# Kernel tuning notes

Measured on AMD Instinct MI355X. Metric: run time of the kernel, lower is better.

The kernel has to match this reference:

```python
import jax, jax.numpy as jnp
import numpy as np

N = 50000   # nodes
E = 800000  # edges (before self-loops)
D = 256     # hidden_dim
H = 8       # heads
C = D // H  # 32 channels per head
NEG_SLOPE = 0.2


def setup_inputs() -> dict:
    key = jax.random.key(0)
    ks = jax.random.split(key, 10)
    sc = 0.05
    x = jax.random.normal(ks[0], (N, D), dtype=jnp.float32)
    edges_idx = jax.random.randint(ks[1], (2, E), 0, N, dtype=jnp.int64)
    # GATv2Conv params per layer: lin_l (W for source j), lin_r (W for target i), att [H,C], bias [H*C]
    Wl1 = jax.random.normal(ks[2], (D, H * C), dtype=jnp.float32) * sc
    Wr1 = jax.random.normal(ks[3], (D, H * C), dtype=jnp.float32) * sc
    att1 = jax.random.normal(ks[4], (H, C), dtype=jnp.float32) * sc
    b1 = jnp.zeros((H * C,), dtype=jnp.float32)
    Wl2 = jax.random.normal(ks[5], (D, H * C), dtype=jnp.float32) * sc
    Wr2 = jax.random.normal(ks[6], (D, H * C), dtype=jnp.float32) * sc
    att2 = jax.random.normal(ks[7], (H, C), dtype=jnp.float32) * sc
    b2 = jnp.zeros((H * C,), dtype=jnp.float32)
    return dict(x=x, edges_idx=edges_idx, Wl1=Wl1, Wr1=Wr1, att1=att1, b1=b1,
                Wl2=Wl2, Wr2=Wr2, att2=att2, b2=b2)


def gatv2_layer(x, src, dst, Wl, Wr, att, b):
    # x: [N, D]; src/dst: [E'] (self-loops included)
    xl = (x @ Wl).reshape(-1, H, C)  # source-side transform
    xr = (x @ Wr).reshape(-1, H, C)  # target-side transform
    # GATv2 score: e_ij = a^T LeakyReLU(Wl x_j + Wr x_i)
    z = jax.nn.leaky_relu(xl[src] + xr[dst], NEG_SLOPE)   # [E', H, C]
    e = jnp.einsum('ehc,hc->eh', z, att)                  # [E', H]
    # softmax over edges sharing the same target node (segment softmax)
    m = jax.ops.segment_max(e, dst, num_segments=N)       # [N, H]
    ex = jnp.exp(e - m[dst])
    s = jax.ops.segment_sum(ex, dst, num_segments=N)      # [N, H]
    alpha = ex / s[dst]                                   # [E', H]
    out = jax.ops.segment_sum(alpha[..., None] * xl[src], dst, num_segments=N)  # [N, H, C]
    return out.reshape(-1, H * C) + b


def reference(x, edges_idx, Wl1, Wr1, att1, b1, Wl2, Wr2, att2, b2):
    # PyG default add_self_loops=True
    loop = jnp.arange(N, dtype=edges_idx.dtype)
    src = jnp.concatenate([edges_idx[0], loop])
    dst = jnp.concatenate([edges_idx[1], loop])
    # layer 1 -> ELU -> layer 2 (dropout identity in eval mode)
    h = jax.nn.elu(gatv2_layer(x, src, dst, Wl1, Wr1, att1, b1))
    return gatv2_layer(h, src, dst, Wl2, Wr2, att2, b2)
```

## Files before the change

### kernel.cpp

```cpp
#include <hip/hip_runtime.h>
#include <hip/hip_bf16.h>
#include <math.h>

#define HEADS 8
#define HC 256
#define NEG_SLOPE 0.2f

typedef __attribute__((ext_vector_type(8))) short short8;
typedef __attribute__((ext_vector_type(16))) float floatx16;

__device__ inline ushort bf16_rne(float f) {
    unsigned u = __float_as_uint(f);
    return (ushort)((u + 0x7FFFu + ((u >> 16) & 1u)) >> 16);
}
__device__ inline float bf2f(ushort u) {
    return __uint_as_float(((unsigned)u) << 16);
}

__global__ __launch_bounds__(256) void cvt_bf16_sw(
        const float* __restrict__ x, ushort* __restrict__ xb, long long nblk) {
    long long id = (long long)blockIdx.x * blockDim.x + threadIdx.x;
    if (id >= nblk) return;
    long long r = id >> 5;
    int j = (int)(id & 31);
    const float4* p = (const float4*)(x + id * 8);
    float4 a = p[0], b = p[1];
    short8 pk;
    pk[0] = (short)bf16_rne(a.x); pk[1] = (short)bf16_rne(a.y);
    pk[2] = (short)bf16_rne(a.z); pk[3] = (short)bf16_rne(a.w);
    pk[4] = (short)bf16_rne(b.x); pk[5] = (short)bf16_rne(b.y);
    pk[6] = (short)bf16_rne(b.z); pk[7] = (short)bf16_rne(b.w);
    int jx = j ^ ((int)r & 7);
    *(short8*)(xb + r * 256 + jx * 8) = pk;
}

__global__ __launch_bounds__(256) void build_wt(
        const float* __restrict__ Wl, const float* __restrict__ Wr,
        ushort* __restrict__ wt) {
    int n = blockIdx.x;
    int k = threadIdx.x;
    const float* W = (n < 256) ? Wl : Wr;
    int col = n & 255;
    int jx = (k >> 3) ^ (n & 7);
    wt[n * HC + jx * 8 + (k & 7)] = bf16_rne(W[k * HC + col]);
}

__global__ __launch_bounds__(256) void gemm_mfma(
        const ushort* __restrict__ A, const ushort* __restrict__ wt,
        ushort* __restrict__ xl, ushort* __restrict__ xr, int N) {
    __shared__ ushort lA[64 * 256];
    __shared__ ushort lB[64 * 256];
    int nt = blockIdx.x & 7;
    int mt = blockIdx.x >> 3;
    int m0 = mt * 64, n0 = nt * 64;
    int t = threadIdx.x;
    int lane = t & 63, wv = t >> 6;

    {
        const ushort* gA = A + (long long)m0 * HC;
        const ushort* gB = wt + (long long)n0 * HC;
        #pragma unroll
        for (int i = 0; i < 8; ++i) {
            int off = (wv * 8 + i) * 512;
            __builtin_amdgcn_global_load_lds(
                (const __attribute__((address_space(1))) unsigned int*)(gA + off + lane * 8),
                (__attribute__((address_space(3))) unsigned int*)(lA + off), 16, 0, 0);
            __builtin_amdgcn_global_load_lds(
                (const __attribute__((address_space(1))) unsigned int*)(gB + off + lane * 8),
                (__attribute__((address_space(3))) unsigned int*)(lB + off), 16, 0, 0);
        }
    }
    __syncthreads();

    int rA = (wv & 1) * 32 + (lane & 31);
    int rB = (wv >> 1) * 32 + (lane & 31);
    int kh = lane >> 5;
    int sA = rA & 7, sB = rB & 7;
    floatx16 acc;
    #pragma unroll
    for (int i = 0; i < 16; ++i) acc[i] = 0.f;
    #pragma unroll
    for (int step = 0; step < 16; ++step) {
        int j = step * 2 + kh;
        short8 a = *(const short8*)&lA[rA * 256 + ((j ^ sA) * 8)];
        short8 b = *(const short8*)&lB[rB * 256 + ((j ^ sB) * 8)];
        acc = __builtin_amdgcn_mfma_f32_32x32x16_bf16(a, b, acc, 0, 0, 0);
    }

    ushort* obase = (nt < 4) ? xl : xr;
    int colb = (n0 & 255) + (wv >> 1) * 32 + (lane & 31);
    int rbase = m0 + (wv & 1) * 32 + 4 * kh;
    #pragma unroll
    for (int g = 0; g < 4; ++g) {
        #pragma unroll
        for (int q = 0; q < 4; ++q) {
            int row = rbase + q + 8 * g;
            if (row < N)
                obase[(long long)row * HC + colb] = bf16_rne(acc[g * 4 + q]);
        }
    }
}

__global__ void hist_dst(const int* __restrict__ eidx, int E, int N,
                         int* __restrict__ counts) {
    int w = blockIdx.x * blockDim.x + threadIdx.x;
    int Etot = E + N;
    if (w >= Etot) return;
    int d = (w < E) ? eidx[E + w] : (w - E);
    atomicAdd(&counts[d], 1);
}

__global__ __launch_bounds__(1024) void scan_local(
        const int* __restrict__ counts, int* __restrict__ rowptr,
        int* __restrict__ bsum, int N) {
    __shared__ int wsums[16];
    int t = threadIdx.x, lane = t & 63, wv = t >> 6;
    int i = blockIdx.x * 1024 + t;
    int v = (i < N) ? counts[i] : 0;
    int orig = v;
    #pragma unroll
    for (int off = 1; off < 64; off <<= 1) {
        int n = __shfl_up(v, off, 64);
        if (lane >= off) v += n;
    }
    if (lane == 63) wsums[wv] = v;
    __syncthreads();
    int woff = 0, total = 0;
    #pragma unroll
    for (int w_ = 0; w_ < 16; ++w_) {
        int s = wsums[w_];
        if (w_ < wv) woff += s;
        total += s;
    }
    if (i < N) rowptr[i] = v + woff - orig;
    if (t == 0) bsum[blockIdx.x] = total;
}

__global__ void scan_bsums(const int* __restrict__ bsum, int* __restrict__ bsum2,
                           int* __restrict__ rowptr, int nb, int N) {
    int lane = threadIdx.x;
    int v = (lane < nb) ? bsum[lane] : 0;
    int orig = v;
    #pragma unroll
    for (int off = 1; off < 64; off <<= 1) {
        int n = __shfl_up(v, off, 64);
        if (lane >= off) v += n;
    }
    if (lane < nb) bsum2[lane] = v - orig;
    if (lane == 63) rowptr[N] = v;
}

__global__ __launch_bounds__(1024) void scan_add(
        int* __restrict__ rowptr, const int* __restrict__ bsum2, int N) {
    int i = blockIdx.x * 1024 + threadIdx.x;
    if (i < N) rowptr[i] += bsum2[blockIdx.x];
}

__global__ void scatter_edges(const int* __restrict__ eidx, int E, int N,
                              const int* __restrict__ rowptr,
                              int* __restrict__ fill, int* __restrict__ srcS) {
    int w = blockIdx.x * blockDim.x + threadIdx.x;
    int Etot = E + N;
    if (w >= Etot) return;
    int s, d;
    if (w < E) { s = eidx[w]; d = eidx[E + w]; }
    else       { s = w - E;   d = w - E; }
    int pos = rowptr[d] + atomicAdd(&fill[d], 1);
    srcS[pos] = s;
}

template <int LAYER1>
__global__ __launch_bounds__(256) void gat_node(
        const ushort* __restrict__ xl, const ushort* __restrict__ xr,
        const float* __restrict__ att, const float* __restrict__ bias,
        const int* __restrict__ rowptr, const int* __restrict__ srcS,
        void* __restrict__ outp, int N) {
    int node = blockIdx.x * 4 + (threadIdx.x >> 6);
    int lane = threadIdx.x & 63;
    if (node >= N) return;
    int half = lane >> 5;
    int l = lane & 31;
    int beg = rowptr[node], end = rowptr[node + 1];

    short8 xu = *(const short8*)(xr + (long long)node * HC + l * 8);
    float xv[8];
    #pragma unroll
    for (int c = 0; c < 8; ++c) xv[c] = bf2f((ushort)xu[c]);
    const float4* ap = (const float4*)(att + l * 8);
    float4 a0 = ap[0], a1 = ap[1];
    float av[8] = {a0.x, a0.y, a0.z, a0.w, a1.x, a1.y, a1.z, a1.w};

    float ss = 0.f;
    float acc[8];
    #pragma unroll
    for (int c = 0; c < 8; ++c) acc[c] = 0.f;

    for (int p = beg + half; p < end; p += 2) {
        int s = srcS[p];
        short8 u = *(const short8*)(xl + (long long)s * HC + l * 8);
        float v[8];
        float st0 = 0.f, st1 = 0.f, sa0 = 0.f, sa1 = 0.f;
        #pragma unroll
        for (int c = 0; c < 4; ++c) {
            v[c] = bf2f((ushort)u[c]);
            float tt = v[c] + xv[c];
            st0 = fmaf(av[c], tt, st0);
            sa0 = fmaf(av[c], fabsf(tt), sa0);
        }
        #pragma unroll
        for (int c = 4; c < 8; ++c) {
            v[c] = bf2f((ushort)u[c]);
            float tt = v[c] + xv[c];
            st1 = fmaf(av[c], tt, st1);
            sa1 = fmaf(av[c], fabsf(tt), sa1);
        }
        float part = 0.6f * (st0 + st1) + 0.4f * (sa0 + sa1);
        part += __shfl_xor(part, 1, 64);
        part += __shfl_xor(part, 2, 64);
        float ex = __expf(part);
        ss += ex;
        #pragma unroll
        for (int c = 0; c < 8; ++c) acc[c] = fmaf(ex, v[c], acc[c]);
    }

    ss += __shfl_xor(ss, 32, 64);
    #pragma unroll
    for (int c = 0; c < 8; ++c) acc[c] += __shfl_xor(acc[c], 32, 64);

    float inv = 1.f / ss;
    const float4* bp = (const float4*)(bias + l * 8);
    float4 b0 = bp[0], b1 = bp[1];
    float bb[8] = {b0.x, b0.y, b0.z, b0.w, b1.x, b1.y, b1.z, b1.w};
    float o[8];
    #pragma unroll
    for (int c = 0; c < 8; ++c) o[c] = acc[c] * inv + bb[c];

    if (half == 0) {
        if (LAYER1) {
            short8 pk;
            #pragma unroll
            for (int c = 0; c < 8; ++c) {
                float e = o[c] > 0.f ? o[c] : expm1f(o[c]);
                pk[c] = (short)bf16_rne(e);
            }
            int jx = l ^ (node & 7);
            *(short8*)((ushort*)outp + (long long)node * HC + jx * 8) = pk;
        } else {
            float* po = (float*)outp + (long long)node * HC + l * 8;
            *(float4*)po = make_float4(o[0], o[1], o[2], o[3]);
            *(float4*)(po + 4) = make_float4(o[4], o[5], o[6], o[7]);
        }
    }
}

extern "C" void kernel_launch(void* const* d_in, const int* in_sizes, int n_in,
                              void* d_out, int out_size, void* d_ws, size_t ws_size,
                              hipStream_t stream) {
    const float* x    = (const float*)d_in[0];
    const int*   eidx = (const int*)d_in[1];
    const float* Wl1  = (const float*)d_in[2];
    const float* Wr1  = (const float*)d_in[3];
    const float* att1 = (const float*)d_in[4];
    const float* b1   = (const float*)d_in[5];
    const float* Wl2  = (const float*)d_in[6];
    const float* Wr2  = (const float*)d_in[7];
    const float* att2 = (const float*)d_in[8];
    const float* b2   = (const float*)d_in[9];
    float* out = (float*)d_out;

    const int N = in_sizes[0] / HC;
    const int E = in_sizes[1] / 2;
    const int Etot = E + N;
    const long long NHC = (long long)N * HC;

    ushort* xl   = (ushort*)d_ws;
    ushort* xr   = xl + NHC;
    ushort* hbuf = xr + NHC;
    ushort* xb   = hbuf + NHC;
    ushort* wt1  = xb + NHC;
    ushort* wt2  = wt1 + 512 * HC;
    int* rowptr  = (int*)(wt2 + 512 * HC);
    int* counts  = rowptr + (N + 1);
    int* fill    = counts + N;
    int* bsum    = fill + N;
    int* bsum2   = bsum + 64;
    int* srcS    = bsum2 + 64;

    const int TB = 256;
    dim3 blk(TB);
    int gEdgesT = (Etot + TB - 1) / TB;
    int gGemm   = ((N + 63) / 64) * 8;
    int gNode   = (N + 3) / 4;
    int nb      = (N + 1023) / 1024;
    long long nblk = NHC / 8;
    int gCvt    = (int)((nblk + TB - 1) / TB);

    cvt_bf16_sw<<<gCvt, blk, 0, stream>>>(x, xb, nblk);
    build_wt<<<512, blk, 0, stream>>>(Wl1, Wr1, wt1);
    build_wt<<<512, blk, 0, stream>>>(Wl2, Wr2, wt2);
    hipMemsetAsync(counts, 0, (size_t)2 * N * sizeof(int), stream);
    hist_dst<<<gEdgesT, blk, 0, stream>>>(eidx, E, N, counts);
    scan_local<<<nb, 1024, 0, stream>>>(counts, rowptr, bsum, N);
    scan_bsums<<<1, 64, 0, stream>>>(bsum, bsum2, rowptr, nb, N);
    scan_add<<<nb, 1024, 0, stream>>>(rowptr, bsum2, N);
    scatter_edges<<<gEdgesT, blk, 0, stream>>>(eidx, E, N, rowptr, fill, srcS);

    gemm_mfma<<<gGemm, blk, 0, stream>>>(xb, wt1, xl, xr, N);
    gat_node<1><<<gNode, blk, 0, stream>>>(xl, xr, att1, b1, rowptr, srcS, hbuf, N);

    gemm_mfma<<<gGemm, blk, 0, stream>>>(hbuf, wt2, xl, xr, N);
    gat_node<0><<<gNode, blk, 0, stream>>>(xl, xr, att2, b2, rowptr, srcS, out, N);
}
```

Measured before the change: 457.1 us.

## Process each node with full wave per edge and regroup GEMM tile order

The node aggregation kernel now has all 64 lanes cover one edge row with 4 channels each, instead of two half-waves each handling alternate edges with 8 channels. Edges are unrolled by two with independent accumulators, and the cross-half shuffle reduction is removed. The GEMM block mapping is regrouped so 16 consecutive M-tiles share an N-tile within a 128-block group, aimed at better L2 reuse of weight tiles. The GEMM change relies on the M-tile guard inside the kernel, since the padded grid now launches extra tiles past N.

```diff
diff --git a/kernel.cpp b/kernel.cpp
--- a/kernel.cpp
+++ b/kernel.cpp
@@ -50,8 +50,10 @@
         ushort* __restrict__ xl, ushort* __restrict__ xr, int N) {
     __shared__ ushort lA[64 * 256];
     __shared__ ushort lB[64 * 256];
-    int nt = blockIdx.x & 7;
-    int mt = blockIdx.x >> 3;
+    int local = blockIdx.x & 127;
+    int grp   = blockIdx.x >> 7;
+    int mt = grp * 16 + (local & 15);
+    int nt = local >> 4;
     int m0 = mt * 64, n0 = nt * 64;
     int t = threadIdx.x;
     int lane = t & 63, wv = t >> 6;
@@ -178,78 +180,68 @@
     int node = blockIdx.x * 4 + (threadIdx.x >> 6);
     int lane = threadIdx.x & 63;
     if (node >= N) return;
-    int half = lane >> 5;
-    int l = lane & 31;
     int beg = rowptr[node], end = rowptr[node + 1];
 
-    short8 xu = *(const short8*)(xr + (long long)node * HC + l * 8);
-    float xv[8];
-    #pragma unroll
-    for (int c = 0; c < 8; ++c) xv[c] = bf2f((ushort)xu[c]);
-    const float4* ap = (const float4*)(att + l * 8);
-    float4 a0 = ap[0], a1 = ap[1];
-    float av[8] = {a0.x, a0.y, a0.z, a0.w, a1.x, a1.y, a1.z, a1.w};
-
-    float ss = 0.f;
-    float acc[8];
-    #pragma unroll
-    for (int c = 0; c < 8; ++c) acc[c] = 0.f;
-
-    for (int p = beg + half; p < end; p += 2) {
-        int s = srcS[p];
-        short8 u = *(const short8*)(xl + (long long)s * HC + l * 8);
-        float v[8];
-        float st0 = 0.f, st1 = 0.f, sa0 = 0.f, sa1 = 0.f;
-        #pragma unroll
-        for (int c = 0; c < 4; ++c) {
-            v[c] = bf2f((ushort)u[c]);
-            float tt = v[c] + xv[c];
-            st0 = fmaf(av[c], tt, st0);
-            sa0 = fmaf(av[c], fabsf(tt), sa0);
-        }
-        #pragma unroll
-        for (int c = 4; c < 8; ++c) {
-            v[c] = bf2f((ushort)u[c]);
-            float tt = v[c] + xv[c];
-            st1 = fmaf(av[c], tt, st1);
-            sa1 = fmaf(av[c], fabsf(tt), sa1);
-        }
-        float part = 0.6f * (st0 + st1) + 0.4f * (sa0 + sa1);
-        part += __shfl_xor(part, 1, 64);
-        part += __shfl_xor(part, 2, 64);
-        float ex = __expf(part);
-        ss += ex;
-        #pragma unroll
-        for (int c = 0; c < 8; ++c) acc[c] = fmaf(ex, v[c], acc[c]);
-    }
-
-    ss += __shfl_xor(ss, 32, 64);
-    #pragma unroll
-    for (int c = 0; c < 8; ++c) acc[c] += __shfl_xor(acc[c], 32, 64);
-
-    float inv = 1.f / ss;
-    const float4* bp = (const float4*)(bias + l * 8);
-    float4 b0 = bp[0], b1 = bp[1];
-    float bb[8] = {b0.x, b0.y, b0.z, b0.w, b1.x, b1.y, b1.z, b1.w};
-    float o[8];
-    #pragma unroll
-    for (int c = 0; c < 8; ++c) o[c] = acc[c] * inv + bb[c];
-
-    if (half == 0) {
-        if (LAYER1) {
-            short8 pk;
-            #pragma unroll
-            for (int c = 0; c < 8; ++c) {
-                float e = o[c] > 0.f ? o[c] : expm1f(o[c]);
-                pk[c] = (short)bf16_rne(e);
-            }
-            int jx = l ^ (node & 7);
-            *(short8*)((ushort*)outp + (long long)node * HC + jx * 8) = pk;
-        } else {
-            float* po = (float*)outp + (long long)node * HC + l * 8;
-            *(float4*)po = make_float4(o[0], o[1], o[2], o[3]);
-            *(float4*)(po + 4) = make_float4(o[4], o[5], o[6], o[7]);
-        }
+    ushort4 xu = *(const ushort4*)(xr + (long long)node * HC + lane * 4);
+    float xr0 = bf2f(xu.x), xr1 = bf2f(xu.y), xr2 = bf2f(xu.z), xr3 = bf2f(xu.w);
+    float4 atv = *(const float4*)(att + lane * 4);
+
+    float ssA = 0.f, ssB = 0.f;
+    float4 aA = make_float4(0.f, 0.f, 0.f, 0.f);
+    float4 aB = make_float4(0.f, 0.f, 0.f, 0.f);
+
+#define EDGE_BODY(P, SS, AC)                                                   \
+    {                                                                          \
+        int s = srcS[P];                                                       \
+        ushort4 u = *(const ushort4*)(xl + (long long)s * HC + lane * 4);      \
+        float v0 = bf2f(u.x), v1 = bf2f(u.y), v2 = bf2f(u.z), v3 = bf2f(u.w);  \
+        float t0 = v0 + xr0, t1 = v1 + xr1, t2 = v2 + xr2, t3 = v3 + xr3;      \
+        float st = atv.x * t0;                                                 \
+        st = fmaf(atv.y, t1, st);                                              \
+        st = fmaf(atv.z, t2, st);                                              \
+        st = fmaf(atv.w, t3, st);                                              \
+        float sa = atv.x * fabsf(t0);                                          \
+        sa = fmaf(atv.y, fabsf(t1), sa);                                       \
+        sa = fmaf(atv.z, fabsf(t2), sa);                                       \
+        sa = fmaf(atv.w, fabsf(t3), sa);                                       \
+        float sc = fmaf(0.6f, st, 0.4f * sa);                                  \
+        sc += __shfl_xor(sc, 1, 64);                                           \
+        sc += __shfl_xor(sc, 2, 64);                                           \
+        sc += __shfl_xor(sc, 4, 64);                                           \
+        float ex = __expf(sc);                                                 \
+        SS += ex;                                                              \
+        AC.x = fmaf(ex, v0, AC.x); AC.y = fmaf(ex, v1, AC.y);                  \
+        AC.z = fmaf(ex, v2, AC.z); AC.w = fmaf(ex, v3, AC.w);                  \
+    }
+
+    int p = beg;
+    for (; p + 1 < end; p += 2) {
+        EDGE_BODY(p, ssA, aA)
+        EDGE_BODY(p + 1, ssB, aB)
+    }
+    if (p < end) EDGE_BODY(p, ssA, aA)
+#undef EDGE_BODY
+
+    float inv = 1.f / (ssA + ssB);
+    float4 bv = *(const float4*)(bias + lane * 4);
+    float o0 = (aA.x + aB.x) * inv + bv.x;
+    float o1 = (aA.y + aB.y) * inv + bv.y;
+    float o2 = (aA.z + aB.z) * inv + bv.z;
+    float o3 = (aA.w + aB.w) * inv + bv.w;
+    if (LAYER1) {
+        o0 = o0 > 0.f ? o0 : expm1f(o0);
+        o1 = o1 > 0.f ? o1 : expm1f(o1);
+        o2 = o2 > 0.f ? o2 : expm1f(o2);
+        o3 = o3 > 0.f ? o3 : expm1f(o3);
+        ushort4 pk;
+        pk.x = bf16_rne(o0); pk.y = bf16_rne(o1);
+        pk.z = bf16_rne(o2); pk.w = bf16_rne(o3);
+        int jx = (lane >> 1) ^ (node & 7);
+        *(ushort4*)((ushort*)outp + (long long)node * HC + jx * 8 +
+                    (lane & 1) * 4) = pk;
+    } else {
+        *(float4*)((float*)outp + (long long)node * HC + lane * 4) =
+            make_float4(o0, o1, o2, o3);
     }
 }
 
@@ -289,7 +281,8 @@
     const int TB = 256;
     dim3 blk(TB);
     int gEdgesT = (Etot + TB - 1) / TB;
-    int gGemm   = ((N + 63) / 64) * 8;
+    int mtTiles = (N + 63) / 64;
+    int gGemm   = ((mtTiles + 15) / 16) * 128;
     int gNode   = (N + 3) / 4;
     int nb      = (N + 1023) / 1024;
     long long nblk = NHC / 8;
```

Result: faster. 431.0 us (-5.7%).
